# Performance work log

Measured on AMD Instinct MI355X. Metric: run time of the kernel, lower is better.

## Reference

```python
import jax, jax.numpy as jnp
import numpy as np

B, S, D, H = 4, 2048, 1024, 16
HD = D // H  # head_dim = 64
SCALE = 1.0 / np.sqrt(HD)
NEG = -1e9


def setup_inputs() -> dict:
    key = jax.random.key(0)
    ks = jax.random.split(key, 8)
    return {
        "query": jax.random.normal(ks[0], (B, S, D), jnp.float32),
        "key": jax.random.normal(ks[1], (B, S, D), jnp.float32),
        "value": jax.random.normal(ks[2], (B, S, D), jnp.float32),
        "mask": jax.random.randint(ks[3], (B, 1, S, S), 0, 2, jnp.int32),
        "Wq": jax.random.normal(ks[4], (D, D), jnp.float32) * 0.02,
        "Wk": jax.random.normal(ks[5], (D, D), jnp.float32) * 0.02,
        "Wv": jax.random.normal(ks[6], (D, D), jnp.float32) * 0.02,
        "Wo": jax.random.normal(ks[7], (D, D), jnp.float32) * 0.02,
    }


def _split_heads(x):
    # [B,S,D] -> [B,H,S,HD]
    b, s, _ = x.shape
    return x.reshape(b, s, H, HD).transpose(0, 2, 1, 3)


def reference(query, key, value, mask, Wq, Wk, Wv, Wo):
    # nn.Linear(d,d,bias=False): y = x @ W.T ; here Wq etc. are the weight matrices.
    q = _split_heads(query @ Wq.T)
    k = _split_heads(key @ Wk.T)
    v = _split_heads(value @ Wv.T)
    scores = jnp.einsum("bhqd,bhkd->bhqk", q, k) * SCALE
    scores = jnp.where(mask == 0, NEG, scores)
    probs = jax.nn.softmax(scores, axis=-1)  # dropout p=0 (eval) -> identity
    attn = jnp.einsum("bhqk,bhkd->bhqd", probs, v)
    attn = attn.transpose(0, 2, 1, 3).reshape(query.shape[0], query.shape[1], D)
    return attn @ Wo.T
```

## Files before the change

### kernel.cpp

```cpp
#include <hip/hip_runtime.h>
#include <hip/hip_bf16.h>
#include <stdint.h>


typedef unsigned short u16;
typedef __bf16  bf16x8 __attribute__((ext_vector_type(8)));
typedef float   fx4    __attribute__((ext_vector_type(4)));
typedef u16     u16x4v __attribute__((ext_vector_type(4)));
typedef u16     u16x8v __attribute__((ext_vector_type(8)));

#define MFMA16(a, b, c) __builtin_amdgcn_mfma_f32_16x16x32_bf16(a, b, c, 0, 0, 0)

__device__ __forceinline__ u16 f2bf(float f) {
    __bf16 b = (__bf16)f;
    return __builtin_bit_cast(unsigned short, b);
}

__device__ __forceinline__ void gload_lds16(const void* g, void* l) {
    auto gp = (const __attribute__((address_space(1))) unsigned int*)(uintptr_t)g;
    auto lp = (__attribute__((address_space(3))) unsigned int*)(unsigned int)(uintptr_t)l;
    __builtin_amdgcn_global_load_lds(gp, lp, 16, 0, 0);
}

__global__ __launch_bounds__(256) void cast3_k(const float* __restrict__ s0,
                                               const float* __restrict__ s1,
                                               const float* __restrict__ s2,
                                               u16* __restrict__ d0,
                                               u16* __restrict__ d1,
                                               u16* __restrict__ d2, int n8) {
    int i = blockIdx.x * 256 + threadIdx.x;
    if (i >= n8) return;
    const float* s = (blockIdx.y == 0) ? s0 : (blockIdx.y == 1) ? s1 : s2;
    u16* d = (blockIdx.y == 0) ? d0 : (blockIdx.y == 1) ? d1 : d2;
    const float4* s4 = (const float4*)s;
    float4 a = s4[(size_t)i * 2];
    float4 b = s4[(size_t)i * 2 + 1];
    u16x8v o;
    o[0] = f2bf(a.x); o[1] = f2bf(a.y); o[2] = f2bf(a.z); o[3] = f2bf(a.w);
    o[4] = f2bf(b.x); o[5] = f2bf(b.y); o[6] = f2bf(b.z); o[7] = f2bf(b.w);
    *(u16x8v*)(d + (size_t)i * 8) = o;
}

__global__ __launch_bounds__(256) void castw_k(const float* __restrict__ s0,
                                               const float* __restrict__ s1,
                                               const float* __restrict__ s2,
                                               const float* __restrict__ s3,
                                               u16* __restrict__ d0,
                                               u16* __restrict__ d1,
                                               u16* __restrict__ d2,
                                               u16* __restrict__ d3, int n8) {
    int i = blockIdx.x * 256 + threadIdx.x;
    if (i >= n8) return;
    const float* s = (blockIdx.y == 0) ? s0 : (blockIdx.y == 1) ? s1
                   : (blockIdx.y == 2) ? s2 : s3;
    u16* d = (blockIdx.y == 0) ? d0 : (blockIdx.y == 1) ? d1
           : (blockIdx.y == 2) ? d2 : d3;
    float sc = (blockIdx.y == 0) ? 0.1803368801111204f : 1.0f;
    const float4* s4 = (const float4*)s;
    float4 a = s4[(size_t)i * 2];
    float4 b = s4[(size_t)i * 2 + 1];
    u16x8v o;
    o[0] = f2bf(a.x * sc); o[1] = f2bf(a.y * sc); o[2] = f2bf(a.z * sc); o[3] = f2bf(a.w * sc);
    o[4] = f2bf(b.x * sc); o[5] = f2bf(b.y * sc); o[6] = f2bf(b.z * sc); o[7] = f2bf(b.w * sc);
    *(u16x8v*)(d + (size_t)i * 8) = o;
}

__global__ __launch_bounds__(256) void pack_mask_k(const int* __restrict__ m,
                                                   unsigned long long* __restrict__ o,
                                                   int nw) {
    int t = blockIdx.x * 256 + threadIdx.x;
    int wid = t >> 6;
    if (wid >= nw) return;
    int v = m[(size_t)wid * 64 + (t & 63)];
    unsigned long long bits = __ballot(v != 0);
    if ((t & 63) == 0) o[wid] = bits;
}

template <int MODE>
__global__ __launch_bounds__(256) void gemm_bt(const u16* __restrict__ A,
                                               const u16* __restrict__ Bw,
                                               void* __restrict__ Cp,
                                               int M, int N, int K) {
    __shared__ __align__(16) u16 As[128 * 32];
    __shared__ __align__(16) u16 Bs[128 * 32];
    const int tid = threadIdx.x;
    const int w = tid >> 6, l = tid & 63, lg = l >> 4, lr = l & 15;
    const int wr = w >> 1, wc = w & 1;
    const int nb = N >> 7;
    const int bm = blockIdx.x / nb, bn = blockIdx.x % nb;

    fx4 acc[4][4] = {};

    const int id0 = tid, id1 = 256 + tid;
    const int r0 = id0 >> 2, k80 = (id0 & 3) * 8;
    const int r1 = id1 >> 2, k81 = (id1 & 3) * 8;
    const u16* Ab = A + (size_t)(bm * 128) * K;
    const u16* Bb = Bw + (size_t)(bn * 128) * K;
    char* AsW0 = (char*)As + (w * 64) * 16;
    char* AsW1 = (char*)As + (256 + w * 64) * 16;
    char* BsW0 = (char*)Bs + (w * 64) * 16;
    char* BsW1 = (char*)Bs + (256 + w * 64) * 16;

    for (int k0 = 0; k0 < K; k0 += 32) {
        __syncthreads();
        gload_lds16(Ab + (size_t)r0 * K + k0 + k80, AsW0);
        gload_lds16(Ab + (size_t)r1 * K + k0 + k81, AsW1);
        gload_lds16(Bb + (size_t)r0 * K + k0 + k80, BsW0);
        gload_lds16(Bb + (size_t)r1 * K + k0 + k81, BsW1);
        __syncthreads();
        bf16x8 af[4], bf[4];
#pragma unroll
        for (int m = 0; m < 4; ++m)
            af[m] = *(const bf16x8*)(As + (wr * 64 + m * 16 + lr) * 32 + lg * 8);
#pragma unroll
        for (int n = 0; n < 4; ++n)
            bf[n] = *(const bf16x8*)(Bs + (wc * 64 + n * 16 + lr) * 32 + lg * 8);
#pragma unroll
        for (int m = 0; m < 4; ++m)
#pragma unroll
            for (int n = 0; n < 4; ++n)
                acc[m][n] = MFMA16(af[m], bf[n], acc[m][n]);
    }

    if (MODE == 2) {
        float* Cf = (float*)Cp;
#pragma unroll
        for (int m = 0; m < 4; ++m) {
#pragma unroll
            for (int n = 0; n < 4; ++n) {
                int c = bn * 128 + wc * 64 + n * 16 + lr;
#pragma unroll
                for (int j = 0; j < 4; ++j) {
                    int r = bm * 128 + wr * 64 + m * 16 + lg * 4 + j;
                    Cf[(size_t)r * N + c] = acc[m][n][j];
                }
            }
        }
    } else if (MODE == 0) {
        u16* Cb = (u16*)Cp;
#pragma unroll
        for (int m = 0; m < 4; ++m) {
#pragma unroll
            for (int n = 0; n < 4; ++n) {
                int c = bn * 128 + wc * 64 + n * 16 + lr;
                int hh = c >> 6, hd = c & 63;
#pragma unroll
                for (int j = 0; j < 4; ++j) {
                    int r = bm * 128 + wr * 64 + m * 16 + lg * 4 + j;
                    int bb = r >> 11, s = r & 2047;
                    Cb[((size_t)(bb * 16 + hh) * 2048 + s) * 64 + hd] =
                        f2bf(acc[m][n][j]);
                }
            }
        }
    } else {
        u16* Cb = (u16*)Cp;
#pragma unroll
        for (int m = 0; m < 4; ++m) {
            int rb = bm * 128 + wr * 64 + m * 16 + lg * 4;
            int bb = rb >> 11, s0 = rb & 2047;
#pragma unroll
            for (int n = 0; n < 4; ++n) {
                int c = bn * 128 + wc * 64 + n * 16 + lr;
                int hh = c >> 6, hd = c & 63;
                u16x4v pk;
#pragma unroll
                for (int j = 0; j < 4; ++j) pk[j] = f2bf(acc[m][n][j]);
                *(u16x4v*)(Cb + ((size_t)(bb * 16 + hh) * 64 + hd) * 2048 + s0) = pk;
            }
        }
    }
}

__global__ __launch_bounds__(256) void attn_k(const u16* __restrict__ qh,
                                              const u16* __restrict__ kh,
                                              const u16* __restrict__ vt,
                                              const unsigned long long* __restrict__ mb,
                                              u16* __restrict__ out) {
    __shared__ __align__(16) u16 Ks[64 * 64];
    __shared__ __align__(16) u16 Vs[64 * 64];
    __shared__ __align__(16) u16 Ps[4][16 * 64];

    const int tid = threadIdx.x;
    const int w = tid >> 6, l = tid & 63, lg = l >> 4, lr = l & 15;
    const int lg4 = lg * 4;
    const int qt = blockIdx.x;
    const int bh = blockIdx.y;
    const int bb = bh >> 4, hh = bh & 15;

    const u16* qp = qh + (size_t)bh * 2048 * 64;
    const u16* kp = kh + (size_t)bh * 2048 * 64;
    const u16* vp = vt + (size_t)bh * 64 * 2048;
    const unsigned long long* mbp = mb + (size_t)bb * 2048 * 32;

    const int qrow0 = qt * 64 + w * 16;
    const int qrow = qrow0 + lr;

    bf16x8 qf[2];
    qf[0] = *(const bf16x8*)(qp + (size_t)qrow * 64 + lg * 8);
    qf[1] = *(const bf16x8*)(qp + (size_t)qrow * 64 + 32 + lg * 8);

    fx4 accO[4] = {};
    float mrun = -INFINITY;
    float lrun = 0.f;

    u16* pw = Ps[w];
    const int swl = (lr & 7) << 4;

    const int sr0 = tid >> 3,        sc0 = (tid & 7) * 8;
    const int sr1 = (256 + tid) >> 3, sc1 = (tid & 7) * 8;
    const int lb0 = sr0 * 128 + ((sc0 * 2) ^ ((sr0 & 7) << 4));
    const int lb1 = sr1 * 128 + ((sc1 * 2) ^ ((sr1 & 7) << 4));

    bf16x8 kr0 = *(const bf16x8*)(kp + (size_t)sr0 * 64 + sc0);
    bf16x8 kr1 = *(const bf16x8*)(kp + (size_t)sr1 * 64 + sc1);
    bf16x8 vr0 = *(const bf16x8*)(vp + (size_t)sr0 * 2048 + sc0);
    bf16x8 vr1 = *(const bf16x8*)(vp + (size_t)sr1 * 2048 + sc1);

    for (int kt = 0; kt < 32; ++kt) {
        uint2 mw = *(const uint2*)(mbp + (size_t)qrow * 32 + kt);

        __syncthreads();
        *(bf16x8*)((char*)Ks + lb0) = kr0;
        *(bf16x8*)((char*)Ks + lb1) = kr1;
        *(bf16x8*)((char*)Vs + lb0) = vr0;
        *(bf16x8*)((char*)Vs + lb1) = vr1;
        __syncthreads();

        if (kt < 31) {
            const u16* kpn = kp + (size_t)(kt + 1) * 64 * 64;
            kr0 = *(const bf16x8*)(kpn + (size_t)sr0 * 64 + sc0);
            kr1 = *(const bf16x8*)(kpn + (size_t)sr1 * 64 + sc1);
            vr0 = *(const bf16x8*)(vp + (size_t)sr0 * 2048 + (kt + 1) * 64 + sc0);
            vr1 = *(const bf16x8*)(vp + (size_t)sr1 * 2048 + (kt + 1) * 64 + sc1);
        }

        fx4 sa[4];
#pragma unroll
        for (int nf = 0; nf < 4; ++nf) {
            int kk = nf * 16 + lr;
            int rb = kk * 128, sw = (kk & 7) << 4;
            fx4 a = {0.f, 0.f, 0.f, 0.f};
            a = MFMA16(*(const bf16x8*)((const char*)Ks + rb + ((lg * 16) ^ sw)), qf[0], a);
            a = MFMA16(*(const bf16x8*)((const char*)Ks + rb + ((64 + lg * 16) ^ sw)), qf[1], a);
            sa[nf] = a;
        }

        float m01 = fmaxf(fmaxf(sa[0][0], sa[0][1]), fmaxf(sa[0][2], sa[0][3]));
        float m23 = fmaxf(fmaxf(sa[1][0], sa[1][1]), fmaxf(sa[1][2], sa[1][3]));
        float m45 = fmaxf(fmaxf(sa[2][0], sa[2][1]), fmaxf(sa[2][2], sa[2][3]));
        float m67 = fmaxf(fmaxf(sa[3][0], sa[3][1]), fmaxf(sa[3][2], sa[3][3]));
        float mt = fmaxf(fmaxf(m01, m23), fmaxf(m45, m67));
        mt = fmaxf(mt, __shfl_xor(mt, 16));
        mt = fmaxf(mt, __shfl_xor(mt, 32));

        if (!__all(mt <= mrun + 8.f)) {
            float mnew = fmaxf(mrun, mt);
            float f = exp2f(mrun - mnew);
            lrun *= f;
            mrun = mnew;
#pragma unroll
            for (int j = 0; j < 4; ++j) {
                float fj = __shfl(f, lg4 + j);
#pragma unroll
                for (int ff = 0; ff < 4; ++ff) accO[ff][j] *= fj;
            }
        }

        float psn[4];
#pragma unroll
        for (int nf = 0; nf < 4; ++nf) {
            unsigned wv = (nf & 2) ? mw.y : mw.x;
            int pos0 = (nf & 1) * 16 + lg4;
            float pv[4];
#pragma unroll
            for (int r = 0; r < 4; ++r) {
                float p = exp2f(sa[nf][r] - mrun);
                int keep = __builtin_amdgcn_sbfe((int)wv, pos0 + r, 1);
                pv[r] = __builtin_bit_cast(float,
                            __builtin_bit_cast(int, p) & keep);
            }
            psn[nf] = (pv[0] + pv[1]) + (pv[2] + pv[3]);
            u16x4v pk;
            pk[0] = f2bf(pv[0]); pk[1] = f2bf(pv[1]);
            pk[2] = f2bf(pv[2]); pk[3] = f2bf(pv[3]);
            *(u16x4v*)((char*)pw + lr * 128 + ((nf * 32 + lg4 * 2) ^ swl)) = pk;
        }
        float ps = (psn[0] + psn[1]) + (psn[2] + psn[3]);
        ps += __shfl_xor(ps, 16);
        ps += __shfl_xor(ps, 32);
        lrun += ps;

#pragma unroll
        for (int ks = 0; ks < 2; ++ks) {
            int pb = lr * 128 + ((ks * 64 + lg * 16) ^ swl);
            bf16x8 pa = *(const bf16x8*)((const char*)pw + pb);
#pragma unroll
            for (int f = 0; f < 4; ++f) {
                int d = f * 16 + lr;
                int vb = d * 128 + ((ks * 64 + lg * 16) ^ ((d & 7) << 4));
                bf16x8 vv = *(const bf16x8*)((const char*)Vs + vb);
                accO[f] = MFMA16(pa, vv, accO[f]);
            }
        }
    }

#pragma unroll
    for (int j = 0; j < 4; ++j) {
        float lj = __shfl(lrun, lg4 + j);
        float rinv = 1.0f / lj;
        int s = qrow0 + lg4 + j;
#pragma unroll
        for (int f = 0; f < 4; ++f) {
            float o = accO[f][j] * rinv;
            out[(size_t)(bb * 2048 + s) * 1024 + hh * 64 + f * 16 + lr] = f2bf(o);
        }
    }
}

extern "C" void kernel_launch(void* const* d_in, const int* in_sizes, int n_in,
                              void* d_out, int out_size, void* d_ws, size_t ws_size,
                              hipStream_t stream) {
    const float* Qin = (const float*)d_in[0];
    const float* Kin = (const float*)d_in[1];
    const float* Vin = (const float*)d_in[2];
    const int*   Mk  = (const int*)d_in[3];
    const float* Wq  = (const float*)d_in[4];
    const float* Wk  = (const float*)d_in[5];
    const float* Wv  = (const float*)d_in[6];
    const float* Wo  = (const float*)d_in[7];

    const size_t NX = (size_t)4 * 2048 * 1024;
    const size_t NW = (size_t)1024 * 1024;

    char* ws = (char*)d_ws;
    size_t off = 0;
    auto carve = [&](size_t bytes) -> char* {
        char* p = ws + off;
        off += (bytes + 255) & ~(size_t)255;
        return p;
    };
    u16* xq = (u16*)carve(NX * 2);
    u16* xk = (u16*)carve(NX * 2);
    u16* xv = (u16*)carve(NX * 2);
    u16* wq = (u16*)carve(NW * 2);
    u16* wk = (u16*)carve(NW * 2);
    u16* wv = (u16*)carve(NW * 2);
    u16* wo = (u16*)carve(NW * 2);
    u16* qh = (u16*)carve(NX * 2);
    u16* kh = (u16*)carve(NX * 2);
    u16* vtb = (u16*)carve(NX * 2);
    unsigned long long* mbits = (unsigned long long*)carve((size_t)4 * 2048 * 32 * 8);
    u16* am = (u16*)carve(NX * 2);

    cast3_k<<<dim3(4096, 3), 256, 0, stream>>>(Qin, Kin, Vin, xq, xk, xv,
                                               (int)(NX / 8));
    castw_k<<<dim3(512, 4), 256, 0, stream>>>(Wq, Wk, Wv, Wo, wq, wk, wv, wo,
                                              (int)(NW / 8));
    pack_mask_k<<<65536, 256, 0, stream>>>(Mk, mbits, 4 * 2048 * 32);

    gemm_bt<0><<<512, 256, 0, stream>>>(xq, wq, qh, 8192, 1024, 1024);
    gemm_bt<0><<<512, 256, 0, stream>>>(xk, wk, kh, 8192, 1024, 1024);
    gemm_bt<1><<<512, 256, 0, stream>>>(xv, wv, vtb, 8192, 1024, 1024);

    attn_k<<<dim3(32, 64), 256, 0, stream>>>(qh, kh, vtb, mbits, am);

    gemm_bt<2><<<512, 256, 0, stream>>>(am, wo, d_out, 8192, 1024, 1024);
}
```

Measured before the change: 496.0 us.

## Process two query sub-tiles per wave in attention and swizzle block indices for XCD locality

Each attention wave now handles 32 query rows as two 16-row sub-tiles, so every K/V fragment read from LDS is reused across both sub-tiles, and the block count drops to 1024 with 128-row query tiles. The row-sum of probabilities is now computed with an MFMA against a ones vector instead of shuffle reductions. Both the attention and GEMM kernels remap block indices so that neighbouring blocks on the same XCD share data. In exchange the attention kernel uses more registers and LDS per block, which may reduce occupancy, and the row sum is taken from the bf16-rounded probabilities.

```diff
diff --git a/kernel.cpp b/kernel.cpp
--- a/kernel.cpp
+++ b/kernel.cpp
@@ -87,7 +87,9 @@
     const int w = tid >> 6, l = tid & 63, lg = l >> 4, lr = l & 15;
     const int wr = w >> 1, wc = w & 1;
     const int nb = N >> 7;
-    const int bm = blockIdx.x / nb, bn = blockIdx.x % nb;
+    const int nwg = gridDim.x;
+    const int sw = (blockIdx.x & 7) * (nwg >> 3) + (blockIdx.x >> 3);
+    const int bm = sw / nb, bn = sw % nb;
 
     fx4 acc[4][4] = {};
 
@@ -179,13 +181,14 @@
                                               u16* __restrict__ out) {
     __shared__ __align__(16) u16 Ks[64 * 64];
     __shared__ __align__(16) u16 Vs[64 * 64];
-    __shared__ __align__(16) u16 Ps[4][16 * 64];
+    __shared__ __align__(16) u16 Ps[4][32 * 64];
 
     const int tid = threadIdx.x;
     const int w = tid >> 6, l = tid & 63, lg = l >> 4, lr = l & 15;
     const int lg4 = lg * 4;
-    const int qt = blockIdx.x;
-    const int bh = blockIdx.y;
+    const int sw0 = (blockIdx.x & 7) * 128 + (blockIdx.x >> 3);
+    const int qt = sw0 & 15;
+    const int bh = sw0 >> 4;
     const int bb = bh >> 4, hh = bh & 15;
 
     const u16* qp = qh + (size_t)bh * 2048 * 64;
@@ -193,21 +196,29 @@
     const u16* vp = vt + (size_t)bh * 64 * 2048;
     const unsigned long long* mbp = mb + (size_t)bb * 2048 * 32;
 
-    const int qrow0 = qt * 64 + w * 16;
-    const int qrow = qrow0 + lr;
-
-    bf16x8 qf[2];
-    qf[0] = *(const bf16x8*)(qp + (size_t)qrow * 64 + lg * 8);
-    qf[1] = *(const bf16x8*)(qp + (size_t)qrow * 64 + 32 + lg * 8);
-
-    fx4 accO[4] = {};
-    float mrun = -INFINITY;
-    float lrun = 0.f;
+    const int qrow0 = qt * 128 + w * 32;
+
+    bf16x8 qf[2][2];
+#pragma unroll
+    for (int st = 0; st < 2; ++st) {
+        const u16* qr = qp + (size_t)(qrow0 + st * 16 + lr) * 64;
+        qf[st][0] = *(const bf16x8*)(qr + lg * 8);
+        qf[st][1] = *(const bf16x8*)(qr + 32 + lg * 8);
+    }
+
+    fx4 accO[2][4] = {};
+    fx4 lsum[2] = {};
+    float mrun[2] = {-INFINITY, -INFINITY};
+
+    u16x8v ov;
+#pragma unroll
+    for (int i = 0; i < 8; ++i) ov[i] = 0x3F80;
+    const bf16x8 ones = __builtin_bit_cast(bf16x8, ov);
 
     u16* pw = Ps[w];
     const int swl = (lr & 7) << 4;
 
-    const int sr0 = tid >> 3,        sc0 = (tid & 7) * 8;
+    const int sr0 = tid >> 3,         sc0 = (tid & 7) * 8;
     const int sr1 = (256 + tid) >> 3, sc1 = (tid & 7) * 8;
     const int lb0 = sr0 * 128 + ((sc0 * 2) ^ ((sr0 & 7) << 4));
     const int lb1 = sr1 * 128 + ((sc1 * 2) ^ ((sr1 & 7) << 4));
@@ -218,7 +229,8 @@
     bf16x8 vr1 = *(const bf16x8*)(vp + (size_t)sr1 * 2048 + sc1);
 
     for (int kt = 0; kt < 32; ++kt) {
-        uint2 mw = *(const uint2*)(mbp + (size_t)qrow * 32 + kt);
+        uint2 mw0 = *(const uint2*)(mbp + (size_t)(qrow0 + lr) * 32 + kt);
+        uint2 mw1 = *(const uint2*)(mbp + (size_t)(qrow0 + 16 + lr) * 32 + kt);
 
         __syncthreads();
         *(bf16x8*)((char*)Ks + lb0) = kr0;
@@ -235,85 +247,101 @@
             vr1 = *(const bf16x8*)(vp + (size_t)sr1 * 2048 + (kt + 1) * 64 + sc1);
         }
 
-        fx4 sa[4];
+        fx4 sa[2][4];
 #pragma unroll
         for (int nf = 0; nf < 4; ++nf) {
             int kk = nf * 16 + lr;
             int rb = kk * 128, sw = (kk & 7) << 4;
-            fx4 a = {0.f, 0.f, 0.f, 0.f};
-            a = MFMA16(*(const bf16x8*)((const char*)Ks + rb + ((lg * 16) ^ sw)), qf[0], a);
-            a = MFMA16(*(const bf16x8*)((const char*)Ks + rb + ((64 + lg * 16) ^ sw)), qf[1], a);
-            sa[nf] = a;
-        }
-
-        float m01 = fmaxf(fmaxf(sa[0][0], sa[0][1]), fmaxf(sa[0][2], sa[0][3]));
-        float m23 = fmaxf(fmaxf(sa[1][0], sa[1][1]), fmaxf(sa[1][2], sa[1][3]));
-        float m45 = fmaxf(fmaxf(sa[2][0], sa[2][1]), fmaxf(sa[2][2], sa[2][3]));
-        float m67 = fmaxf(fmaxf(sa[3][0], sa[3][1]), fmaxf(sa[3][2], sa[3][3]));
-        float mt = fmaxf(fmaxf(m01, m23), fmaxf(m45, m67));
-        mt = fmaxf(mt, __shfl_xor(mt, 16));
-        mt = fmaxf(mt, __shfl_xor(mt, 32));
-
-        if (!__all(mt <= mrun + 8.f)) {
-            float mnew = fmaxf(mrun, mt);
-            float f = exp2f(mrun - mnew);
-            lrun *= f;
-            mrun = mnew;
-#pragma unroll
-            for (int j = 0; j < 4; ++j) {
-                float fj = __shfl(f, lg4 + j);
-#pragma unroll
-                for (int ff = 0; ff < 4; ++ff) accO[ff][j] *= fj;
-            }
-        }
-
-        float psn[4];
-#pragma unroll
-        for (int nf = 0; nf < 4; ++nf) {
-            unsigned wv = (nf & 2) ? mw.y : mw.x;
-            int pos0 = (nf & 1) * 16 + lg4;
-            float pv[4];
-#pragma unroll
-            for (int r = 0; r < 4; ++r) {
-                float p = exp2f(sa[nf][r] - mrun);
-                int keep = __builtin_amdgcn_sbfe((int)wv, pos0 + r, 1);
-                pv[r] = __builtin_bit_cast(float,
+            bf16x8 kf0 = *(const bf16x8*)((const char*)Ks + rb + ((lg * 16) ^ sw));
+            bf16x8 kf1 = *(const bf16x8*)((const char*)Ks + rb + ((64 + lg * 16) ^ sw));
+#pragma unroll
+            for (int st = 0; st < 2; ++st) {
+                fx4 a = {0.f, 0.f, 0.f, 0.f};
+                a = MFMA16(kf0, qf[st][0], a);
+                a = MFMA16(kf1, qf[st][1], a);
+                sa[st][nf] = a;
+            }
+        }
+
+        float mt[2];
+#pragma unroll
+        for (int st = 0; st < 2; ++st) {
+            float m01 = fmaxf(fmaxf(sa[st][0][0], sa[st][0][1]), fmaxf(sa[st][0][2], sa[st][0][3]));
+            float m23 = fmaxf(fmaxf(sa[st][1][0], sa[st][1][1]), fmaxf(sa[st][1][2], sa[st][1][3]));
+            float m45 = fmaxf(fmaxf(sa[st][2][0], sa[st][2][1]), fmaxf(sa[st][2][2], sa[st][2][3]));
+            float m67 = fmaxf(fmaxf(sa[st][3][0], sa[st][3][1]), fmaxf(sa[st][3][2], sa[st][3][3]));
+            float m = fmaxf(fmaxf(m01, m23), fmaxf(m45, m67));
+            m = fmaxf(m, __shfl_xor(m, 16));
+            m = fmaxf(m, __shfl_xor(m, 32));
+            mt[st] = m;
+        }
+
+        if (!__all(mt[0] <= mrun[0] + 8.f && mt[1] <= mrun[1] + 8.f)) {
+#pragma unroll
+            for (int st = 0; st < 2; ++st) {
+                float mnew = fmaxf(mrun[st], mt[st]);
+                float f = exp2f(mrun[st] - mnew);
+                mrun[st] = mnew;
+#pragma unroll
+                for (int j = 0; j < 4; ++j) {
+                    float fj = __shfl(f, lg4 + j);
+                    lsum[st][j] *= fj;
+#pragma unroll
+                    for (int ff = 0; ff < 4; ++ff) accO[st][ff][j] *= fj;
+                }
+            }
+        }
+
+#pragma unroll
+        for (int st = 0; st < 2; ++st) {
+            uint2 mw = st ? mw1 : mw0;
+            int rowb = (st * 16 + lr) * 128;
+#pragma unroll
+            for (int nf = 0; nf < 4; ++nf) {
+                unsigned wv = (nf & 2) ? mw.y : mw.x;
+                int pos0 = (nf & 1) * 16 + lg4;
+                u16x4v pk;
+#pragma unroll
+                for (int r = 0; r < 4; ++r) {
+                    float p = exp2f(sa[st][nf][r] - mrun[st]);
+                    int keep = __builtin_amdgcn_sbfe((int)wv, pos0 + r, 1);
+                    p = __builtin_bit_cast(float,
                             __builtin_bit_cast(int, p) & keep);
-            }
-            psn[nf] = (pv[0] + pv[1]) + (pv[2] + pv[3]);
-            u16x4v pk;
-            pk[0] = f2bf(pv[0]); pk[1] = f2bf(pv[1]);
-            pk[2] = f2bf(pv[2]); pk[3] = f2bf(pv[3]);
-            *(u16x4v*)((char*)pw + lr * 128 + ((nf * 32 + lg4 * 2) ^ swl)) = pk;
-        }
-        float ps = (psn[0] + psn[1]) + (psn[2] + psn[3]);
-        ps += __shfl_xor(ps, 16);
-        ps += __shfl_xor(ps, 32);
-        lrun += ps;
+                    pk[r] = f2bf(p);
+                }
+                *(u16x4v*)((char*)pw + rowb + ((nf * 32 + lg4 * 2) ^ swl)) = pk;
+            }
+        }
 
 #pragma unroll
         for (int ks = 0; ks < 2; ++ks) {
-            int pb = lr * 128 + ((ks * 64 + lg * 16) ^ swl);
-            bf16x8 pa = *(const bf16x8*)((const char*)pw + pb);
+            int pco = (ks * 64 + lg * 16);
+            bf16x8 pa0 = *(const bf16x8*)((const char*)pw + lr * 128 + (pco ^ swl));
+            bf16x8 pa1 = *(const bf16x8*)((const char*)pw + (16 + lr) * 128 + (pco ^ swl));
+            lsum[0] = MFMA16(pa0, ones, lsum[0]);
+            lsum[1] = MFMA16(pa1, ones, lsum[1]);
 #pragma unroll
             for (int f = 0; f < 4; ++f) {
                 int d = f * 16 + lr;
-                int vb = d * 128 + ((ks * 64 + lg * 16) ^ ((d & 7) << 4));
+                int vb = d * 128 + (pco ^ ((d & 7) << 4));
                 bf16x8 vv = *(const bf16x8*)((const char*)Vs + vb);
-                accO[f] = MFMA16(pa, vv, accO[f]);
-            }
-        }
-    }
-
-#pragma unroll
-    for (int j = 0; j < 4; ++j) {
-        float lj = __shfl(lrun, lg4 + j);
-        float rinv = 1.0f / lj;
-        int s = qrow0 + lg4 + j;
-#pragma unroll
-        for (int f = 0; f < 4; ++f) {
-            float o = accO[f][j] * rinv;
-            out[(size_t)(bb * 2048 + s) * 1024 + hh * 64 + f * 16 + lr] = f2bf(o);
+                accO[0][f] = MFMA16(pa0, vv, accO[0][f]);
+                accO[1][f] = MFMA16(pa1, vv, accO[1][f]);
+            }
+        }
+    }
+
+#pragma unroll
+    for (int st = 0; st < 2; ++st) {
+#pragma unroll
+        for (int j = 0; j < 4; ++j) {
+            float rinv = 1.0f / lsum[st][j];
+            int s = qrow0 + st * 16 + lg4 + j;
+#pragma unroll
+            for (int f = 0; f < 4; ++f) {
+                float o = accO[st][f][j] * rinv;
+                out[(size_t)(bb * 2048 + s) * 1024 + hh * 64 + f * 16 + lr] = f2bf(o);
+            }
         }
     }
 }
@@ -363,7 +391,7 @@
     gemm_bt<0><<<512, 256, 0, stream>>>(xk, wk, kh, 8192, 1024, 1024);
     gemm_bt<1><<<512, 256, 0, stream>>>(xv, wv, vtb, 8192, 1024, 1024);
 
-    attn_k<<<dim3(32, 64), 256, 0, stream>>>(qh, kh, vtb, mbits, am);
+    attn_k<<<1024, 256, 0, stream>>>(qh, kh, vtb, mbits, am);
 
     gemm_bt<2><<<512, 256, 0, stream>>>(am, wo, d_out, 8192, 1024, 1024);
 }
```

Measured after the change: 484.4 us. -2.3%, faster.
